# Kernel optimization log

Measured on AMD Instinct MI355X. Metric: run time of the kernel, lower is better.

Reference implementation:

```python
import jax, jax.numpy as jnp
import numpy as np

B, C, T = 32, 1024, 1024
BETA = 0.95      # snn.Leaky(beta=0.95)
THR = 1.0        # snntorch Leaky default threshold
SIGMA_INIT = 10.5  # mean of sigma_range (1, 20)


def _gaussian_matrix(sigma, channels):
    # row i is the Gaussian pdf over x=0..C-1 centered at mean=i (vectorized
    # form of the source's per-row Python loop; identical values).
    x = jnp.arange(channels, dtype=jnp.float32)
    u = (x[None, :] - x[:, None]) / sigma  # [C, C]
    coef = 1.0 / (sigma * jnp.sqrt(jnp.asarray(2.0 * jnp.pi, dtype=jnp.float32)))
    return coef * jnp.exp(-0.5 * u * u)


def _spike(u):
    # heaviside(u) forward; ATan surrogate gradient (snntorch default, alpha=2)
    soft = jnp.arctan(jnp.pi * u) / jnp.pi
    hard = (u > 0).astype(u.dtype)
    return soft + jax.lax.stop_gradient(hard - soft)


def setup_inputs() -> dict:
    key = jax.random.key(0)
    inp = jax.random.normal(key, (B, C, T), dtype=jnp.float32)
    sigma = jnp.ones((1,), dtype=jnp.float32) * SIGMA_INIT
    return {"inp": inp, "sigma": sigma}


def reference(inp, sigma):
    # inp: [B, C, T], sigma: [1]
    s = sigma[0]
    w = _gaussian_matrix(s, inp.shape[1])  # computed once: identical at every t
    # I[b,i,t] = x[b,i,t] - sum_j w[i,j] * x[b,j,t]
    I = inp - jnp.einsum('ij,bjt->bit', w, inp)
    I_tbc = jnp.moveaxis(I, 2, 0)  # [T, B, C]

    def step(mem, It):
        # snntorch Leaky (reset_mechanism='subtract'):
        # reset fires on incoming mem, then decay+integrate, then spike.
        reset = _spike(mem - THR)
        mem = BETA * mem + It - reset * THR
        spk = _spike(mem - THR)
        return mem, spk

    mem0 = jnp.zeros(I_tbc.shape[1:], dtype=inp.dtype)  # [B, C]
    _, spks = jax.lax.scan(step, mem0, I_tbc)  # spks: [T, B, C]
    return jnp.moveaxis(spks, 0, 2)  # [B, C, T]
```

## Files before the change

kernel.cpp:

```cpp
#include <hip/hip_runtime.h>
#include <math.h>

#define B_     32
#define C_     1024
#define T_     1024
#define RT     92
#define CT     64
#define TT     64
#define KC     8
#define NTY    8
#define NJQ    48
#define WN     (2*(RT + KC - 1) + 1)
#define WOFF   (RT + KC - 1)
#define NCOLS  (CT + 2*RT)
#define XSTR   252
#define ISTR   68

__device__ __forceinline__ float tap_value(float s, int d) {
    float u    = __fdiv_rn((float)d, s);
    float t1   = __fmul_rn(-0.5f, u);
    float t2   = __fmul_rn(t1, u);
    float e    = (float)exp((double)t2);
    float den  = __fmul_rn(s, sqrtf(6.2831854820251465f));
    float coef = __fdiv_rn(1.0f, den);
    return __fmul_rn(coef, e);
}

__global__ void init_w_kernel(const float* __restrict__ sigma, float* __restrict__ gw) {
    int i = threadIdx.x;
    if (i < WN) {
        int d = i - WOFF;
        gw[i] = (d >= -RT && d <= RT) ? tap_value(sigma[0], d) : 0.0f;
    }
}

template <bool GW>
__global__ __launch_bounds__(512, 4) void snn_v6(
    const float* __restrict__ x, const float* __restrict__ sigma,
    const float* __restrict__ gw, float* __restrict__ out)
{
    __shared__ __align__(16) float xsT[TT * XSTR];
    __shared__ __align__(16) float IsS[NTY * KC * ISTR];

    const int tx   = threadIdx.x;
    const int ty   = threadIdx.y;
    const int flat = ty * 64 + tx;
    const int b    = blockIdx.y;
    const int c0   = blockIdx.x * CT;
    const int rb   = ty * KC;

    const float* xb = x   + (size_t)b * ((size_t)C_ * T_);
    float*       ob = out + (size_t)b * ((size_t)C_ * T_);

    float sv = 0.0f;
    if (!GW) sv = sigma[0];

    float4 stg[2][4];
    const int rB  = (flat >> 2);
    const int c4B = (flat & 3);

#define STAGE_LOAD(T0)                                                          \
    _Pragma("unroll")                                                           \
    for (int i1 = 0; i1 < 2; ++i1) {                                            \
        _Pragma("unroll")                                                       \
        for (int i2 = 0; i2 < 4; ++i2) {                                        \
            int r  = rB + 128 * i1;                                             \
            int c4 = c4B + 4 * i2;                                              \
            int c  = c0 - RT + r;                                               \
            float4 v = make_float4(0.f, 0.f, 0.f, 0.f);                         \
            if (r < NCOLS && c >= 0 && c < C_)                                  \
                v = *(const float4*)(xb + (size_t)c * T_ + (T0) + c4 * 4);      \
            stg[i1][i2] = v;                                                    \
        }                                                                       \
    }

#define STAGE_WRITE()                                                           \
    _Pragma("unroll")                                                           \
    for (int i1 = 0; i1 < 2; ++i1) {                                            \
        _Pragma("unroll")                                                       \
        for (int i2 = 0; i2 < 4; ++i2) {                                        \
            int r  = rB + 128 * i1;                                             \
            int c4 = c4B + 4 * i2;                                              \
            if (r < NCOLS) {                                                    \
                xsT[(4 * c4 + 0) * XSTR + r] = stg[i1][i2].x;                   \
                xsT[(4 * c4 + 1) * XSTR + r] = stg[i1][i2].y;                   \
                xsT[(4 * c4 + 2) * XSTR + r] = stg[i1][i2].z;                   \
                xsT[(4 * c4 + 3) * XSTR + r] = stg[i1][i2].w;                   \
            }                                                                   \
        }                                                                       \
    }

    STAGE_LOAD(0);

    float mem = 0.0f;
    float* strip = IsS + ty * (KC * ISTR);

    for (int kk = 0; kk < T_ / TT; ++kk) {
        const int t0 = kk * TT;

        STAGE_WRITE();
        __syncthreads();

        if (kk < T_ / TT - 1) { STAGE_LOAD(t0 + TT); }

        float acc[KC];
#pragma unroll
        for (int k = 0; k < KC; ++k) acc[k] = 0.0f;

        const float* xrow = &xsT[tx * XSTR + rb];
#pragma unroll 4
        for (int jq = 0; jq < NJQ; ++jq) {
            float4 xv = *(const float4*)(xrow + 4 * jq);
#pragma unroll
            for (int qq = 0; qq < 4; ++qq) {
                float xs1 = (qq == 0) ? xv.x : (qq == 1) ? xv.y : (qq == 2) ? xv.z : xv.w;
#pragma unroll
                for (int k = 0; k < KC; ++k) {
                    float wv;
                    if (GW) {
                        wv = gw[4 * jq + qq + 7 - k];
                    } else {
                        int d = 4 * jq + qq + 7 - k - WOFF;
                        wv = (d >= -RT && d <= RT) ? tap_value(sv, d) : 0.0f;
                    }
                    acc[k] = fmaf(wv, xs1, acc[k]);
                }
            }
        }

        float4 xoA = *(const float4*)(xrow + RT);
        float4 xoB = *(const float4*)(xrow + RT + 4);
        {
            float xo[KC] = {xoA.x, xoA.y, xoA.z, xoA.w, xoB.x, xoB.y, xoB.z, xoB.w};
#pragma unroll
            for (int k = 0; k < KC; ++k)
                strip[k * ISTR + tx] = __fsub_rn(xo[k], acc[k]);
        }

        if (tx < KC) {
            float m = mem;
            const float* srow = strip + tx * ISTR;
            float* orow = ob + (size_t)(c0 + rb + tx) * T_ + t0;
#pragma unroll 4
            for (int q = 0; q < TT / 4; ++q) {
                float4 Iq = *(const float4*)(srow + 4 * q);
                float4 s;
#pragma unroll
                for (int qq = 0; qq < 4; ++qq) {
                    float Ivv = (qq == 0) ? Iq.x : (qq == 1) ? Iq.y : (qq == 2) ? Iq.z : Iq.w;
                    float r   = (m > 1.0f) ? 1.0f : 0.0f;
                    m = __fsub_rn(__fadd_rn(__fmul_rn(0.95f, m), Ivv), r);
                    float sp  = (m > 1.0f) ? 1.0f : 0.0f;
                    if (qq == 0) s.x = sp; else if (qq == 1) s.y = sp;
                    else if (qq == 2) s.z = sp; else s.w = sp;
                }
                *(float4*)(orow + 4 * q) = s;
            }
            mem = m;
        }
        __syncthreads();
    }
#undef STAGE_LOAD
#undef STAGE_WRITE
}

extern "C" void kernel_launch(void* const* d_in, const int* in_sizes, int n_in,
                              void* d_out, int out_size, void* d_ws, size_t ws_size,
                              hipStream_t stream) {
    const float* x     = (const float*)d_in[0];
    const float* sigma = (const float*)d_in[1];
    float* out = (float*)d_out;

    dim3 grid(C_ / CT, B_);
    dim3 block(64, NTY);

    if (ws_size >= WN * sizeof(float)) {
        float* gw = (float*)d_ws;
        init_w_kernel<<<1, 256, 0, stream>>>(sigma, gw);
        snn_v6<true><<<grid, block, 0, stream>>>(x, sigma, gw, out);
    } else {
        snn_v6<false><<<grid, block, 0, stream>>>(x, sigma, nullptr, out);
    }
}
```

Measured before the change: 186.0 us.

## Compute Gaussian taps into shared memory per block and rotate weight registers

After: 217.1 us. +16.7%, slower.

```diff
diff --git a/kernel.cpp b/kernel.cpp
--- a/kernel.cpp
+++ b/kernel.cpp
@@ -12,9 +12,10 @@
 #define NJQ    48
 #define WN     (2*(RT + KC - 1) + 1)
 #define WOFF   (RT + KC - 1)
+#define NWT    208
 #define NCOLS  (CT + 2*RT)
 #define XSTR   252
-#define ISTR   68
+#define ISTR   64
 
 __device__ __forceinline__ float tap_value(float s, int d) {
     float u    = __fdiv_rn((float)d, s);
@@ -26,21 +27,15 @@
     return __fmul_rn(coef, e);
 }
 
-__global__ void init_w_kernel(const float* __restrict__ sigma, float* __restrict__ gw) {
-    int i = threadIdx.x;
-    if (i < WN) {
-        int d = i - WOFF;
-        gw[i] = (d >= -RT && d <= RT) ? tap_value(sigma[0], d) : 0.0f;
-    }
-}
+#define EL(v, i) ((i) == 0 ? (v).x : (i) == 1 ? (v).y : (i) == 2 ? (v).z : (v).w)
 
-template <bool GW>
-__global__ __launch_bounds__(512, 4) void snn_v6(
+__global__ __launch_bounds__(512, 4) void snn_v7(
     const float* __restrict__ x, const float* __restrict__ sigma,
-    const float* __restrict__ gw, float* __restrict__ out)
+    float* __restrict__ out)
 {
     __shared__ __align__(16) float xsT[TT * XSTR];
     __shared__ __align__(16) float IsS[NTY * KC * ISTR];
+    __shared__ __align__(16) float wtab[NWT];
 
     const int tx   = threadIdx.x;
     const int ty   = threadIdx.y;
@@ -49,11 +44,13 @@
     const int c0   = blockIdx.x * CT;
     const int rb   = ty * KC;
 
+    if (flat < NWT) {
+        int d = flat - WOFF;
+        wtab[flat] = (flat < WN && d >= -RT && d <= RT) ? tap_value(sigma[0], d) : 0.0f;
+    }
+
     const float* xb = x   + (size_t)b * ((size_t)C_ * T_);
     float*       ob = out + (size_t)b * ((size_t)C_ * T_);
-
-    float sv = 0.0f;
-    if (!GW) sv = sigma[0];
 
     float4 stg[2][4];
     const int rB  = (flat >> 2);
@@ -90,10 +87,28 @@
         }                                                                       \
     }
 
+#define STEP(JQ, WP, WQ, WR)                                                    \
+    {                                                                           \
+        float4 xv = xrow4[JQ];                                                  \
+        _Pragma("unroll")                                                       \
+        for (int qq = 0; qq < 4; ++qq) {                                        \
+            float x1 = EL(xv, qq);                                              \
+            _Pragma("unroll")                                                   \
+            for (int k = 0; k < KC; ++k) {                                      \
+                const int idx = qq + 7 - k;                                     \
+                float wv = (idx < 4) ? EL(WP, idx)                              \
+                         : (idx < 8) ? EL(WQ, idx - 4) : EL(WR, idx - 8);       \
+                acc[k] = fmaf(wv, x1, acc[k]);                                  \
+            }                                                                   \
+        }                                                                       \
+    }
+
     STAGE_LOAD(0);
 
     float mem = 0.0f;
+    float rc  = 0.0f;
     float* strip = IsS + ty * (KC * ISTR);
+    const float4* wt4 = (const float4*)wtab;
 
     for (int kk = 0; kk < T_ / TT; ++kk) {
         const int t0 = kk * TT;
@@ -107,30 +122,23 @@
 #pragma unroll
         for (int k = 0; k < KC; ++k) acc[k] = 0.0f;
 
-        const float* xrow = &xsT[tx * XSTR + rb];
-#pragma unroll 4
-        for (int jq = 0; jq < NJQ; ++jq) {
-            float4 xv = *(const float4*)(xrow + 4 * jq);
-#pragma unroll
-            for (int qq = 0; qq < 4; ++qq) {
-                float xs1 = (qq == 0) ? xv.x : (qq == 1) ? xv.y : (qq == 2) ? xv.z : xv.w;
-#pragma unroll
-                for (int k = 0; k < KC; ++k) {
-                    float wv;
-                    if (GW) {
-                        wv = gw[4 * jq + qq + 7 - k];
-                    } else {
-                        int d = 4 * jq + qq + 7 - k - WOFF;
-                        wv = (d >= -RT && d <= RT) ? tap_value(sv, d) : 0.0f;
-                    }
-                    acc[k] = fmaf(wv, xs1, acc[k]);
-                }
-            }
+        const float4* xrow4 = (const float4*)(&xsT[tx * XSTR + rb]);
+        float4 wA = wt4[0];
+        float4 wB = wt4[1];
+        float4 wC;
+#pragma unroll 2
+        for (int jq = 0; jq < NJQ; jq += 3) {
+            wC = wt4[jq + 2];
+            STEP(jq + 0, wA, wB, wC);
+            wA = wt4[jq + 3];
+            STEP(jq + 1, wB, wC, wA);
+            wB = wt4[jq + 4];
+            STEP(jq + 2, wC, wA, wB);
         }
 
-        float4 xoA = *(const float4*)(xrow + RT);
-        float4 xoB = *(const float4*)(xrow + RT + 4);
         {
+            float4 xoA = *(const float4*)((const float*)xrow4 + RT);
+            float4 xoB = *(const float4*)((const float*)xrow4 + RT + 4);
             float xo[KC] = {xoA.x, xoA.y, xoA.z, xoA.w, xoB.x, xoB.y, xoB.z, xoB.w};
 #pragma unroll
             for (int k = 0; k < KC; ++k)
@@ -138,7 +146,7 @@
         }
 
         if (tx < KC) {
-            float m = mem;
+            float m = mem, r = rc;
             const float* srow = strip + tx * ISTR;
             float* orow = ob + (size_t)(c0 + rb + tx) * T_ + t0;
 #pragma unroll 4
@@ -147,21 +155,22 @@
                 float4 s;
 #pragma unroll
                 for (int qq = 0; qq < 4; ++qq) {
-                    float Ivv = (qq == 0) ? Iq.x : (qq == 1) ? Iq.y : (qq == 2) ? Iq.z : Iq.w;
-                    float r   = (m > 1.0f) ? 1.0f : 0.0f;
+                    float Ivv = EL(Iq, qq);
                     m = __fsub_rn(__fadd_rn(__fmul_rn(0.95f, m), Ivv), r);
-                    float sp  = (m > 1.0f) ? 1.0f : 0.0f;
+                    float sp = (m > 1.0f) ? 1.0f : 0.0f;
+                    r = sp;
                     if (qq == 0) s.x = sp; else if (qq == 1) s.y = sp;
                     else if (qq == 2) s.z = sp; else s.w = sp;
                 }
                 *(float4*)(orow + 4 * q) = s;
             }
-            mem = m;
+            mem = m; rc = r;
         }
         __syncthreads();
     }
 #undef STAGE_LOAD
 #undef STAGE_WRITE
+#undef STEP
 }
 
 extern "C" void kernel_launch(void* const* d_in, const int* in_sizes, int n_in,
@@ -174,11 +183,5 @@
     dim3 grid(C_ / CT, B_);
     dim3 block(64, NTY);
 
-    if (ws_size >= WN * sizeof(float)) {
-        float* gw = (float*)d_ws;
-        init_w_kernel<<<1, 256, 0, stream>>>(sigma, gw);
-        snn_v6<true><<<grid, block, 0, stream>>>(x, sigma, gw, out);
-    } else {
-        snn_v6<false><<<grid, block, 0, stream>>>(x, sigma, nullptr, out);
-    }
+    snn_v7<<<grid, block, 0, stream>>>(x, sigma, out);
 }
```
